# Optimization experiments

Measured on AMD Instinct MI355X. Metric: run time of the kernel, lower is better.

The kernel has to match this reference:

```python
import jax, jax.numpy as jnp
import numpy as np

B, C, H, W = 2, 256, 64, 64
D = 4  # max dilation ring


def _offsets():
    offs = [(0, 0)]
    for s in range(1, D + 1):
        for a in (-s, 0, s):
            for b in (-s, 0, s):
                if a != 0 or b != 0:
                    offs.append((a, b))
    return np.array(offs, dtype=np.int32)  # (33, 2)


def setup_inputs() -> dict:
    key = jax.random.key(0)
    k1, k2, k3, k4 = jax.random.split(key, 4)
    scale = 1.0 / np.sqrt(C)
    return {
        "Ft": jax.random.normal(k1, (B, C, H, W), dtype=jnp.float32),
        "Ft_epsilon": jax.random.normal(k2, (B, C, H, W), dtype=jnp.float32),
        "Wf": jax.random.normal(k3, (256, C), dtype=jnp.float32) * scale,
        "bf": jnp.zeros((256,), dtype=jnp.float32),
        "Wg": jax.random.normal(k4, (256, C), dtype=jnp.float32) * scale,
        "bg": jnp.zeros((256,), dtype=jnp.float32),
    }


def reference(Ft, Ft_epsilon, Wf, bf, Wg, bg):
    # 1x1 conv embeddings
    Ef = jnp.einsum("bchw,oc->bohw", Ft, Wf) + bf[None, :, None, None]          # f(Ft)
    Eg = jnp.einsum("bchw,oc->bohw", Ft_epsilon, Wg) + bg[None, :, None, None]  # g(Ft_eps)

    offs = _offsets()                                  # (K,2), K=33
    dx = jnp.asarray(offs[:, 0])[:, None, None]        # (K,1,1)
    dy = jnp.asarray(offs[:, 1])[:, None, None]
    xs = jnp.arange(H)[None, :, None] + dx             # (K,H,1)
    ys = jnp.arange(W)[None, None, :] + dy             # (K,1,W)
    valid = ((xs >= 0) & (xs < H)) & ((ys >= 0) & (ys < W))  # (K,H,W)
    xc = jnp.clip(xs, 0, H - 1)
    yc = jnp.clip(ys, 0, W - 1)

    # gather neighbor embeddings and features: (B,C,K,H,W)
    Ef_n = Ef[:, :, xc, yc]
    Ft_n = Ft[:, :, xc, yc]

    # affinity of center embedding with each neighbor embedding
    aff = jnp.einsum("bchw,bckhw->bkhw", Eg, Ef_n)     # (B,K,H,W)
    aff = jnp.where(valid[None], aff, -jnp.inf)        # clip out-of-bounds neighbors
    w = jax.nn.softmax(aff, axis=1)                    # (B,K,H,W); center always valid

    out = jnp.einsum("bkhw,bckhw->bchw", w, Ft_n)      # (B,C,H,W)
    return out
```

## Files before the change

kernel.cpp:

```cpp
#include <hip/hip_runtime.h>
#include <math.h>

typedef __attribute__((ext_vector_type(4))) float f4;

__device__ __forceinline__ int iclamp(int x, int lo, int hi) { return min(max(x, lo), hi); }

__device__ constexpr int DXC[33] = {0, -1,-1,-1,0,0,1,1,1, -2,-2,-2,0,0,2,2,2, -3,-3,-3,0,0,3,3,3, -4,-4,-4,0,0,4,4,4};
__device__ constexpr int DYC[33] = {0, -1,0,1,-1,1,-1,0,1, -2,0,2,-2,2,-2,0,2, -3,0,3,-3,3,-3,0,3, -4,0,4,-4,4,-4,0,4};

__global__ __launch_bounds__(256) void mat_M(
    const float* __restrict__ Wf, const float* __restrict__ Wg,
    const float* __restrict__ bg, float* __restrict__ M, float* __restrict__ r)
{
    __shared__ float Sf[32][33], Sg[32][33];
    __shared__ float Rs[32][9];
    const int c1b = blockIdx.x * 32, c2b = blockIdx.y * 32;
    const int tid = threadIdx.x;
    const int tx = tid & 15, ty = tid >> 4;
    float acc[2][2] = {};
    for (int ko = 0; ko < 256; ko += 32) {
        #pragma unroll
        for (int i = 0; i < 4; ++i) {
            int f = i * 256 + tid, o = f >> 5, c = f & 31;
            Sf[o][c] = Wf[(ko + o) * 256 + c1b + c];
            Sg[o][c] = Wg[(ko + o) * 256 + c2b + c];
        }
        __syncthreads();
        #pragma unroll
        for (int o = 0; o < 32; ++o) {
            float f0 = Sf[o][ty * 2], f1 = Sf[o][ty * 2 + 1];
            float g0 = Sg[o][tx * 2], g1 = Sg[o][tx * 2 + 1];
            acc[0][0] += f0 * g0; acc[0][1] += f0 * g1;
            acc[1][0] += f1 * g0; acc[1][1] += f1 * g1;
        }
        __syncthreads();
    }
    #pragma unroll
    for (int i = 0; i < 2; ++i)
        #pragma unroll
        for (int j = 0; j < 2; ++j)
            M[(size_t)(c1b + ty * 2 + i) * 256 + c2b + tx * 2 + j] = acc[i][j];

    if (blockIdx.y == 0) {
        const int c1l = tid & 31, og = tid >> 5;
        float s = 0.f;
        #pragma unroll 8
        for (int o = og * 32; o < og * 32 + 32; ++o)
            s += Wf[o * 256 + c1b + c1l] * bg[o];
        Rs[c1l][og] = s;
        __syncthreads();
        if (tid < 32) {
            float t = 0.f;
            #pragma unroll
            for (int j = 0; j < 8; ++j) t += Rs[tid][j];
            r[c1b + tid] = t;
        }
    }
}

__global__ __launch_bounds__(256, 2) void gemm_G(
    const float* __restrict__ M, const float* __restrict__ r,
    const float* __restrict__ FtE, float* __restrict__ G)
{
    __shared__ float As[64][68];
    __shared__ float Bs[64][64];

    const int bid = blockIdx.x;
    const int bn = bid & 63, bm = (bid >> 6) & 3, b = bid >> 8;
    const float* X = FtE + (size_t)b * 256 * 4096;
    float* E = G + (size_t)b * 256 * 4096;
    const int tid = threadIdx.x;
    const int tn = tid & 15, tm = tid >> 4;
    const int m0 = bm * 64, n0 = bn * 64;
    float acc[4][4] = {};
    f4 areg[2], breg[2];

    auto loadA = [&](int kk) {
        #pragma unroll
        for (int i = 0; i < 2; ++i) {
            int f = i * 256 + tid, m = f >> 3, cq = f & 7;
            areg[i] = *(const f4*)&M[(m0 + m) * 256 + kk + cq * 4];
        }
    };
    auto loadB = [&](int kk) {
        #pragma unroll
        for (int i = 0; i < 2; ++i) {
            int f = i * 256 + tid, c = f >> 4, n4 = f & 15;
            breg[i] = *(const f4*)&X[(size_t)(kk + c) * 4096 + n0 + n4 * 4];
        }
    };
    auto storeLDS = [&](int buf) {
        #pragma unroll
        for (int i = 0; i < 2; ++i) {
            int f = i * 256 + tid, m = f >> 3, cq = f & 7;
            As[buf * 32 + cq * 4 + 0][m] = areg[i].x;
            As[buf * 32 + cq * 4 + 1][m] = areg[i].y;
            As[buf * 32 + cq * 4 + 2][m] = areg[i].z;
            As[buf * 32 + cq * 4 + 3][m] = areg[i].w;
        }
        #pragma unroll
        for (int i = 0; i < 2; ++i) {
            int f = i * 256 + tid, c = f >> 4, n4 = f & 15;
            *(f4*)&Bs[buf * 32 + c][n4 * 4] = breg[i];
        }
    };

    loadA(0); loadB(0); storeLDS(0);
    __syncthreads();
    for (int ch = 0; ch < 8; ++ch) {
        const int buf = ch & 1;
        if (ch < 7) { loadA((ch + 1) * 32); loadB((ch + 1) * 32); }
        #pragma unroll 4
        for (int k = 0; k < 32; ++k) {
            f4 a  = *(const f4*)&As[buf * 32 + k][tm * 4];
            f4 bb = *(const f4*)&Bs[buf * 32 + k][tn * 4];
            #pragma unroll
            for (int ii = 0; ii < 4; ++ii)
                #pragma unroll
                for (int jj = 0; jj < 4; ++jj)
                    acc[ii][jj] += a[ii] * bb[jj];
        }
        if (ch < 7) storeLDS(buf ^ 1);
        __syncthreads();
    }
    #pragma unroll
    for (int ii = 0; ii < 4; ++ii) {
        int o = m0 + tm * 4 + ii;
        float bvs = r[o];
        f4 v = { acc[ii][0] + bvs, acc[ii][1] + bvs, acc[ii][2] + bvs, acc[ii][3] + bvs };
        *(f4*)&E[(size_t)o * 4096 + n0 + tn * 4] = v;
    }
}

template<int K0, int NK>
__device__ __forceinline__ void aff_accum(const float* __restrict__ base, float* __restrict__ aff)
{
    #pragma unroll
    for (int ch = 0; ch < 8; ++ch) {
        float eg = base[(72 + ch) * 72];
        #pragma unroll
        for (int j = 0; j < NK; ++j) {
            constexpr int kk0 = K0;
            int k = kk0 + j;
            aff[j] += eg * base[((DXC[k] + 4) * 8 + ch) * 72 + DYC[k]];
        }
    }
}

__global__ __launch_bounds__(256, 2) void aff_part(
    const float* __restrict__ Ftg, const float* __restrict__ Gc,
    float* __restrict__ part)
{
    __shared__ float L[2][10 * 8 * 72];

    const int h = blockIdx.x, b = blockIdx.y, cseg = blockIdx.z;
    const int tid = threadIdx.x;
    const int w = tid & 63, kg = tid >> 6;
    const size_t plane = (size_t)b * 256 * 4096;
    const float* FtB = Ftg + plane;
    const float* GB  = Gc + plane;
    const int cbase = cseg * 64;

    int hr[10];
    #pragma unroll
    for (int d = 0; d < 10; ++d) hr[d] = (d < 9) ? iclamp(h + d - 4, 0, 63) : h;

    f4 vreg[5]; float sreg[3];

    auto load_rnd = [&](int rr) {
        const int c0 = cbase + rr * 8;
        #pragma unroll
        for (int i = 0; i < 5; ++i) {
            int f = i * 256 + tid, d = f >> 7, rem = f & 127, ch = rem >> 4, c4 = rem & 15;
            const float* src = (d < 9) ? FtB : GB;
            vreg[i] = *(const f4*)&src[(size_t)(c0 + ch) * 4096 + hr[d] * 64 + c4 * 4];
        }
        #pragma unroll
        for (int i = 0; i < 3; ++i) {
            int e = i * 256 + tid;
            if (e < 640) {
                int row = e >> 3, sc = e & 7, d = row >> 3, ch = row & 7;
                int wsrc = (sc < 4) ? 0 : 63;
                const float* src = (d < 9) ? FtB : GB;
                sreg[i] = src[(size_t)(c0 + ch) * 4096 + hr[d] * 64 + wsrc];
            }
        }
    };
    auto store_rnd = [&](int buf) {
        float* Lb = L[buf];
        #pragma unroll
        for (int i = 0; i < 5; ++i) {
            int f = i * 256 + tid, d = f >> 7, rem = f & 127, ch = rem >> 4, c4 = rem & 15;
            *(f4*)&Lb[(d * 8 + ch) * 72 + 4 + c4 * 4] = vreg[i];
        }
        #pragma unroll
        for (int i = 0; i < 3; ++i) {
            int e = i * 256 + tid;
            if (e < 640) {
                int row = e >> 3, sc = e & 7, d = row >> 3, ch = row & 7;
                int col = (sc < 4) ? sc : (64 + sc);
                Lb[(d * 8 + ch) * 72 + col] = sreg[i];
            }
        }
    };

    float aff[9] = {0.f,0.f,0.f,0.f,0.f,0.f,0.f,0.f,0.f};

    load_rnd(0); store_rnd(0);
    for (int rr = 0; rr < 8; ++rr) {
        if (rr < 7) load_rnd(rr + 1);
        __syncthreads();
        const float* base = &L[rr & 1][4 + w];
        switch (kg) {
            case 0: aff_accum<0, 9>(base, aff); break;
            case 1: aff_accum<9, 8>(base, aff); break;
            case 2: aff_accum<17, 8>(base, aff); break;
            default: aff_accum<25, 8>(base, aff); break;
        }
        if (rr < 7) store_rnd((rr + 1) & 1);
    }

    const int k0 = (kg == 0) ? 0 : (kg == 1) ? 9 : (kg == 2) ? 17 : 25;
    const int nk = (kg == 0) ? 9 : 8;
    float* pB = part + (((size_t)cseg * 2 + b) * 33) * 4096 + h * 64 + w;
    #pragma unroll
    for (int j = 0; j < 9; ++j)
        if (j < nk) pB[(size_t)(k0 + j) * 4096] = aff[j];
}

__global__ __launch_bounds__(256, 2) void out_kernel(
    const float* __restrict__ part, const float* __restrict__ Ft,
    float* __restrict__ out)
{
    __shared__ float L[2][9 * 8 * 72];

    const int h = blockIdx.x, b = blockIdx.y, cseg = blockIdx.z;
    const int tid = threadIdx.x;
    const int w = tid & 63, cg = tid >> 6;
    const size_t plane = (size_t)b * 256 * 4096;
    const float* FtB = Ft + plane;
    float* outB = out + plane;
    const int cbase = cseg * 64;
    const int p = h * 64 + w;

    int hr[9];
    #pragma unroll
    for (int d = 0; d < 9; ++d) hr[d] = iclamp(h + d - 4, 0, 63);

    f4 vreg[5]; float sreg[3];

    auto load_rnd = [&](int rr) {
        const int c0 = cbase + rr * 8;
        #pragma unroll
        for (int i = 0; i < 5; ++i) {
            int f = i * 256 + tid;
            if (f < 1152) {
                int d = f >> 7, rem = f & 127, ch = rem >> 4, c4 = rem & 15;
                vreg[i] = *(const f4*)&FtB[(size_t)(c0 + ch) * 4096 + hr[d] * 64 + c4 * 4];
            }
        }
        #pragma unroll
        for (int i = 0; i < 3; ++i) {
            int e = i * 256 + tid;
            if (e < 576) {
                int row = e >> 3, sc = e & 7, d = row >> 3, ch = row & 7;
                int wsrc = (sc < 4) ? 0 : 63;
                sreg[i] = FtB[(size_t)(c0 + ch) * 4096 + hr[d] * 64 + wsrc];
            }
        }
    };
    auto store_rnd = [&](int buf) {
        float* Lb = L[buf];
        #pragma unroll
        for (int i = 0; i < 5; ++i) {
            int f = i * 256 + tid;
            if (f < 1152) {
                int d = f >> 7, rem = f & 127, ch = rem >> 4, c4 = rem & 15;
                *(f4*)&Lb[(d * 8 + ch) * 72 + 4 + c4 * 4] = vreg[i];
            }
        }
        #pragma unroll
        for (int i = 0; i < 3; ++i) {
            int e = i * 256 + tid;
            if (e < 576) {
                int row = e >> 3, sc = e & 7, d = row >> 3, ch = row & 7;
                int col = (sc < 4) ? sc : (64 + sc);
                Lb[(d * 8 + ch) * 72 + col] = sreg[i];
            }
        }
    };

    load_rnd(0);

    float wv[33];
    {
        constexpr size_t CS = (size_t)2 * 33 * 4096;
        const float* pB = part + ((size_t)b * 33) * 4096 + p;
        float mx = -INFINITY;
        #pragma unroll
        for (int k = 0; k < 33; ++k) {
            size_t off = (size_t)k * 4096;
            float s = pB[off] + pB[CS + off] + pB[2 * CS + off] + pB[3 * CS + off];
            bool valid = ((unsigned)(h + DXC[k]) < 64u) && ((unsigned)(w + DYC[k]) < 64u);
            wv[k] = valid ? s : -INFINITY;
            mx = fmaxf(mx, wv[k]);
        }
        float ssum = 0.f;
        #pragma unroll
        for (int k = 0; k < 33; ++k) { float e = __expf(wv[k] - mx); wv[k] = e; ssum += e; }
        float inv = 1.0f / ssum;
        #pragma unroll
        for (int k = 0; k < 33; ++k) wv[k] *= inv;
    }

    store_rnd(0);
    for (int rr = 0; rr < 8; ++rr) {
        if (rr < 7) load_rnd(rr + 1);
        __syncthreads();
        const float* base = &L[rr & 1][4 + w];
        #pragma unroll
        for (int u = 0; u < 2; ++u) {
            const float* b2 = base + (cg * 2 + u) * 72;
            float o = 0.f;
            #pragma unroll
            for (int k = 0; k < 33; ++k)
                o += wv[k] * b2[(DXC[k] + 4) * 576 + DYC[k]];
            int c = cbase + rr * 8 + cg * 2 + u;
            outB[(size_t)c * 4096 + p] = o;
        }
        if (rr < 7) store_rnd((rr + 1) & 1);
    }
}

extern "C" void kernel_launch(void* const* d_in, const int* in_sizes, int n_in,
                              void* d_out, int out_size, void* d_ws, size_t ws_size,
                              hipStream_t stream) {
    const float* Ft  = (const float*)d_in[0];
    const float* FtE = (const float*)d_in[1];
    const float* Wf  = (const float*)d_in[2];
    const float* bf  = (const float*)d_in[3];
    const float* Wg  = (const float*)d_in[4];
    const float* bg  = (const float*)d_in[5];
    float* out = (float*)d_out;
    (void)bf;

    float* G    = (float*)d_ws;
    float* part = G + (size_t)2 * 256 * 4096;
    float* Mw   = part + (size_t)4 * 2 * 33 * 4096;
    float* rw   = Mw + 256 * 256;

    hipLaunchKernelGGL(mat_M,      dim3(8, 8),     dim3(256), 0, stream, Wf, Wg, bg, Mw, rw);
    hipLaunchKernelGGL(gemm_G,     dim3(512),      dim3(256), 0, stream, Mw, rw, FtE, G);
    hipLaunchKernelGGL(aff_part,   dim3(64, 2, 4), dim3(256), 0, stream, Ft, G, part);
    hipLaunchKernelGGL(out_kernel, dim3(64, 2, 4), dim3(256), 0, stream, part, Ft, out);
}
```

Baseline: 141.0 us.

## Drop LDS tiling in gemm_G and register-block affinity over pixel quads

mat_M now writes M transposed so that gemm_G can read f4 columns of A directly from global memory. gemm_G drops its LDS double-buffered tiling in favour of a plain register-blocked 4x4 outer-product loop over k that relies on caches. aff_part is remapped so each thread handles four consecutive pixels and a subset of offsets for two channels. It loads neighbour windows as f4 from LDS and reduces across channel groups with cross-lane shuffles. The goal is fewer LDS reads and better reuse in the affinity stage, at the cost of more global and cache traffic in the GEMM.

```diff
diff --git a/kernel.cpp b/kernel.cpp
--- a/kernel.cpp
+++ b/kernel.cpp
@@ -10,7 +10,7 @@
 
 __global__ __launch_bounds__(256) void mat_M(
     const float* __restrict__ Wf, const float* __restrict__ Wg,
-    const float* __restrict__ bg, float* __restrict__ M, float* __restrict__ r)
+    const float* __restrict__ bg, float* __restrict__ Mt, float* __restrict__ r)
 {
     __shared__ float Sf[32][33], Sg[32][33];
     __shared__ float Rs[32][9];
@@ -39,7 +39,7 @@
     for (int i = 0; i < 2; ++i)
         #pragma unroll
         for (int j = 0; j < 2; ++j)
-            M[(size_t)(c1b + ty * 2 + i) * 256 + c2b + tx * 2 + j] = acc[i][j];
+            Mt[(size_t)(c2b + tx * 2 + j) * 256 + c1b + ty * 2 + i] = acc[i][j];
 
     if (blockIdx.y == 0) {
         const int c1l = tid & 31, og = tid >> 5;
@@ -58,91 +58,91 @@
     }
 }
 
-__global__ __launch_bounds__(256, 2) void gemm_G(
-    const float* __restrict__ M, const float* __restrict__ r,
+__global__ __launch_bounds__(256) void gemm_G(
+    const float* __restrict__ Mt, const float* __restrict__ r,
     const float* __restrict__ FtE, float* __restrict__ G)
 {
-    __shared__ float As[64][68];
-    __shared__ float Bs[64][64];
-
     const int bid = blockIdx.x;
     const int bn = bid & 63, bm = (bid >> 6) & 3, b = bid >> 8;
-    const float* X = FtE + (size_t)b * 256 * 4096;
-    float* E = G + (size_t)b * 256 * 4096;
     const int tid = threadIdx.x;
     const int tn = tid & 15, tm = tid >> 4;
-    const int m0 = bm * 64, n0 = bn * 64;
-    float acc[4][4] = {};
-    f4 areg[2], breg[2];
-
-    auto loadA = [&](int kk) {
-        #pragma unroll
-        for (int i = 0; i < 2; ++i) {
-            int f = i * 256 + tid, m = f >> 3, cq = f & 7;
-            areg[i] = *(const f4*)&M[(m0 + m) * 256 + kk + cq * 4];
-        }
-    };
-    auto loadB = [&](int kk) {
-        #pragma unroll
-        for (int i = 0; i < 2; ++i) {
-            int f = i * 256 + tid, c = f >> 4, n4 = f & 15;
-            breg[i] = *(const f4*)&X[(size_t)(kk + c) * 4096 + n0 + n4 * 4];
-        }
-    };
-    auto storeLDS = [&](int buf) {
-        #pragma unroll
-        for (int i = 0; i < 2; ++i) {
-            int f = i * 256 + tid, m = f >> 3, cq = f & 7;
-            As[buf * 32 + cq * 4 + 0][m] = areg[i].x;
-            As[buf * 32 + cq * 4 + 1][m] = areg[i].y;
-            As[buf * 32 + cq * 4 + 2][m] = areg[i].z;
-            As[buf * 32 + cq * 4 + 3][m] = areg[i].w;
-        }
-        #pragma unroll
-        for (int i = 0; i < 2; ++i) {
-            int f = i * 256 + tid, c = f >> 4, n4 = f & 15;
-            *(f4*)&Bs[buf * 32 + c][n4 * 4] = breg[i];
-        }
-    };
-
-    loadA(0); loadB(0); storeLDS(0);
-    __syncthreads();
-    for (int ch = 0; ch < 8; ++ch) {
-        const int buf = ch & 1;
-        if (ch < 7) { loadA((ch + 1) * 32); loadB((ch + 1) * 32); }
-        #pragma unroll 4
-        for (int k = 0; k < 32; ++k) {
-            f4 a  = *(const f4*)&As[buf * 32 + k][tm * 4];
-            f4 bb = *(const f4*)&Bs[buf * 32 + k][tn * 4];
-            #pragma unroll
-            for (int ii = 0; ii < 4; ++ii)
-                #pragma unroll
-                for (int jj = 0; jj < 4; ++jj)
-                    acc[ii][jj] += a[ii] * bb[jj];
-        }
-        if (ch < 7) storeLDS(buf ^ 1);
-        __syncthreads();
-    }
-    #pragma unroll
-    for (int ii = 0; ii < 4; ++ii) {
-        int o = m0 + tm * 4 + ii;
-        float bvs = r[o];
-        f4 v = { acc[ii][0] + bvs, acc[ii][1] + bvs, acc[ii][2] + bvs, acc[ii][3] + bvs };
-        *(f4*)&E[(size_t)o * 4096 + n0 + tn * 4] = v;
-    }
-}
-
-template<int K0, int NK>
-__device__ __forceinline__ void aff_accum(const float* __restrict__ base, float* __restrict__ aff)
-{
-    #pragma unroll
-    for (int ch = 0; ch < 8; ++ch) {
-        float eg = base[(72 + ch) * 72];
-        #pragma unroll
-        for (int j = 0; j < NK; ++j) {
-            constexpr int kk0 = K0;
-            int k = kk0 + j;
-            aff[j] += eg * base[((DXC[k] + 4) * 8 + ch) * 72 + DYC[k]];
+    const int m0g = bm * 64 + tm * 4;
+    const int n0g = bn * 64 + tn * 4;
+    const float* A = Mt + m0g;
+    const float* X = FtE + (size_t)b * 1048576 + n0g;
+
+    f4 acc0 = {0.f,0.f,0.f,0.f}, acc1 = acc0, acc2 = acc0, acc3 = acc0;
+
+    #pragma unroll 8
+    for (int k = 0; k < 256; ++k) {
+        f4 a = *(const f4*)(A + (size_t)k * 256);
+        f4 x = *(const f4*)(X + (size_t)k * 4096);
+        acc0 += x * a.x;
+        acc1 += x * a.y;
+        acc2 += x * a.z;
+        acc3 += x * a.w;
+    }
+
+    float* Gp = G + (size_t)b * 1048576;
+    {
+        f4 v;
+        v = acc0 + r[m0g + 0]; *(f4*)&Gp[(size_t)(m0g + 0) * 4096 + n0g] = v;
+        v = acc1 + r[m0g + 1]; *(f4*)&Gp[(size_t)(m0g + 1) * 4096 + n0g] = v;
+        v = acc2 + r[m0g + 2]; *(f4*)&Gp[(size_t)(m0g + 2) * 4096 + n0g] = v;
+        v = acc3 + r[m0g + 3]; *(f4*)&Gp[(size_t)(m0g + 3) * 4096 + n0g] = v;
+    }
+}
+
+template<bool LO, bool HI>
+__device__ __forceinline__ void ldwin(float* wn, const float* Lb, int rd, int ch, int wq) {
+    const float* p = &Lb[(rd * 8 + ch) * 72 + wq * 4];
+    if constexpr (LO) { f4 v = *(const f4*)p;       wn[0]=v.x; wn[1]=v.y; wn[2]=v.z;  wn[3]=v.w; }
+    {                   f4 v = *(const f4*)(p + 4); wn[4]=v.x; wn[5]=v.y; wn[6]=v.z;  wn[7]=v.w; }
+    if constexpr (HI) { f4 v = *(const f4*)(p + 8); wn[8]=v.x; wn[9]=v.y; wn[10]=v.z; wn[11]=v.w; }
+}
+
+template<int DY>
+__device__ __forceinline__ void fmadd4(f4& a, const f4& eg, const float* wn) {
+    a.x += eg.x * wn[4 + DY];
+    a.y += eg.y * wn[5 + DY];
+    a.z += eg.z * wn[6 + DY];
+    a.w += eg.w * wn[7 + DY];
+}
+
+template<int KQ>
+__device__ __forceinline__ void aff_compute(const float* Lb, int wq, int cg, f4* acc)
+{
+    #pragma unroll
+    for (int chi = 0; chi < 2; ++chi) {
+        const int ch = cg * 2 + chi;
+        f4 eg = *(const f4*)&Lb[(72 + ch) * 72 + 4 + wq * 4];
+        float wn[12];
+        if constexpr (KQ == 0) {
+            ldwin<true,true>(wn, Lb, 0, ch, wq);
+            fmadd4<-4>(acc[0], eg, wn); fmadd4<0>(acc[1], eg, wn); fmadd4<4>(acc[2], eg, wn);
+            ldwin<true,true>(wn, Lb, 1, ch, wq);
+            fmadd4<-3>(acc[3], eg, wn); fmadd4<0>(acc[4], eg, wn); fmadd4<3>(acc[5], eg, wn);
+            ldwin<true,true>(wn, Lb, 2, ch, wq);
+            fmadd4<-2>(acc[6], eg, wn); fmadd4<0>(acc[7], eg, wn); fmadd4<2>(acc[8], eg, wn);
+        } else if constexpr (KQ == 1) {
+            ldwin<true,true>(wn, Lb, 3, ch, wq);
+            fmadd4<-1>(acc[0], eg, wn); fmadd4<0>(acc[1], eg, wn); fmadd4<1>(acc[2], eg, wn);
+            ldwin<true,false>(wn, Lb, 4, ch, wq);
+            fmadd4<-1>(acc[3], eg, wn); fmadd4<-2>(acc[4], eg, wn);
+            fmadd4<-3>(acc[5], eg, wn); fmadd4<-4>(acc[6], eg, wn);
+        } else if constexpr (KQ == 2) {
+            ldwin<false,true>(wn, Lb, 4, ch, wq);
+            fmadd4<0>(acc[0], eg, wn); fmadd4<1>(acc[1], eg, wn); fmadd4<2>(acc[2], eg, wn);
+            fmadd4<3>(acc[3], eg, wn); fmadd4<4>(acc[4], eg, wn);
+            ldwin<true,true>(wn, Lb, 5, ch, wq);
+            fmadd4<-1>(acc[5], eg, wn); fmadd4<0>(acc[6], eg, wn); fmadd4<1>(acc[7], eg, wn);
+        } else {
+            ldwin<true,true>(wn, Lb, 6, ch, wq);
+            fmadd4<-2>(acc[0], eg, wn); fmadd4<0>(acc[1], eg, wn); fmadd4<2>(acc[2], eg, wn);
+            ldwin<true,true>(wn, Lb, 7, ch, wq);
+            fmadd4<-3>(acc[3], eg, wn); fmadd4<0>(acc[4], eg, wn); fmadd4<3>(acc[5], eg, wn);
+            ldwin<true,true>(wn, Lb, 8, ch, wq);
+            fmadd4<-4>(acc[6], eg, wn); fmadd4<0>(acc[7], eg, wn); fmadd4<4>(acc[8], eg, wn);
         }
     }
 }
@@ -155,7 +155,7 @@
 
     const int h = blockIdx.x, b = blockIdx.y, cseg = blockIdx.z;
     const int tid = threadIdx.x;
-    const int w = tid & 63, kg = tid >> 6;
+    const int wq = tid & 15, cg = (tid >> 4) & 3, kq = tid >> 6;
     const size_t plane = (size_t)b * 256 * 4096;
     const float* FtB = Ftg + plane;
     const float* GB  = Gc + plane;
@@ -204,28 +204,41 @@
         }
     };
 
-    float aff[9] = {0.f,0.f,0.f,0.f,0.f,0.f,0.f,0.f,0.f};
+    f4 acc[9] = {};
 
     load_rnd(0); store_rnd(0);
     for (int rr = 0; rr < 8; ++rr) {
         if (rr < 7) load_rnd(rr + 1);
         __syncthreads();
-        const float* base = &L[rr & 1][4 + w];
-        switch (kg) {
-            case 0: aff_accum<0, 9>(base, aff); break;
-            case 1: aff_accum<9, 8>(base, aff); break;
-            case 2: aff_accum<17, 8>(base, aff); break;
-            default: aff_accum<25, 8>(base, aff); break;
+        const float* Lb = L[rr & 1];
+        switch (kq) {
+            case 0: aff_compute<0>(Lb, wq, cg, acc); break;
+            case 1: aff_compute<1>(Lb, wq, cg, acc); break;
+            case 2: aff_compute<2>(Lb, wq, cg, acc); break;
+            default: aff_compute<3>(Lb, wq, cg, acc); break;
         }
         if (rr < 7) store_rnd((rr + 1) & 1);
     }
 
-    const int k0 = (kg == 0) ? 0 : (kg == 1) ? 9 : (kg == 2) ? 17 : 25;
-    const int nk = (kg == 0) ? 9 : 8;
-    float* pB = part + (((size_t)cseg * 2 + b) * 33) * 4096 + h * 64 + w;
-    #pragma unroll
-    for (int j = 0; j < 9; ++j)
-        if (j < nk) pB[(size_t)(k0 + j) * 4096] = aff[j];
+    #pragma unroll
+    for (int j = 0; j < 9; ++j) {
+        acc[j].x += __shfl_xor(acc[j].x, 16); acc[j].x += __shfl_xor(acc[j].x, 32);
+        acc[j].y += __shfl_xor(acc[j].y, 16); acc[j].y += __shfl_xor(acc[j].y, 32);
+        acc[j].z += __shfl_xor(acc[j].z, 16); acc[j].z += __shfl_xor(acc[j].z, 32);
+        acc[j].w += __shfl_xor(acc[j].w, 16); acc[j].w += __shfl_xor(acc[j].w, 32);
+    }
+
+    if (cg == 0) {
+        float* pB = part + (((size_t)cseg * 2 + b) * 33) * 4096 + h * 64 + wq * 4;
+        #define STP(K, J) *(f4*)&pB[(size_t)(K) * 4096] = acc[J];
+        switch (kq) {
+            case 0: STP(25,0) STP(26,1) STP(27,2) STP(17,3) STP(18,4) STP(19,5) STP(9,6) STP(10,7) STP(11,8) break;
+            case 1: STP(1,0) STP(2,1) STP(3,2) STP(4,3) STP(12,4) STP(20,5) STP(28,6) break;
+            case 2: STP(0,0) STP(5,1) STP(13,2) STP(21,3) STP(29,4) STP(6,5) STP(7,6) STP(8,7) break;
+            default: STP(14,0) STP(15,1) STP(16,2) STP(22,3) STP(23,4) STP(24,5) STP(30,6) STP(31,7) STP(32,8) break;
+        }
+        #undef STP
+    }
 }
 
 __global__ __launch_bounds__(256, 2) void out_kernel(
@@ -346,11 +359,11 @@
 
     float* G    = (float*)d_ws;
     float* part = G + (size_t)2 * 256 * 4096;
-    float* Mw   = part + (size_t)4 * 2 * 33 * 4096;
-    float* rw   = Mw + 256 * 256;
-
-    hipLaunchKernelGGL(mat_M,      dim3(8, 8),     dim3(256), 0, stream, Wf, Wg, bg, Mw, rw);
-    hipLaunchKernelGGL(gemm_G,     dim3(512),      dim3(256), 0, stream, Mw, rw, FtE, G);
+    float* Mt   = part + (size_t)4 * 2 * 33 * 4096;
+    float* rw   = Mt + 256 * 256;
+
+    hipLaunchKernelGGL(mat_M,      dim3(8, 8),     dim3(256), 0, stream, Wf, Wg, bg, Mt, rw);
+    hipLaunchKernelGGL(gemm_G,     dim3(512),      dim3(256), 0, stream, Mt, rw, FtE, G);
     hipLaunchKernelGGL(aff_part,   dim3(64, 2, 4), dim3(256), 0, stream, Ft, G, part);
     hipLaunchKernelGGL(out_kernel, dim3(64, 2, 4), dim3(256), 0, stream, part, Ft, out);
 }
```

Result: slower. 161.4 us (+14.4%).
